# Optimization experiments

Measured on AMD Instinct MI355X. Metric: run time of the kernel, lower is better.

## Reference

```python
import jax, jax.numpy as jnp
import numpy as np

N = 100000   # nodes
E = 1250000  # edges
G = 64       # graphs in batch
F_IN, H, NT, GT = 29, 64, 6, 4
L = 4        # num GCN layers


def setup_inputs() -> dict:
    key = jax.random.key(0)
    ks = jax.random.split(key, 14)
    s_in = 1.0 / np.sqrt(F_IN)
    s_h = 1.0 / np.sqrt(H)
    return {
        "x": jax.random.normal(ks[0], (N, F_IN), dtype=jnp.float32),
        "edge_index": jax.random.randint(ks[1], (2, E), 0, N, dtype=jnp.int64),
        "batch": jnp.sort(jax.random.randint(ks[2], (N,), 0, G, dtype=jnp.int64)),
        "encW": jax.random.uniform(ks[3], (F_IN, H), jnp.float32, -s_in, s_in),
        "encb": jax.random.uniform(ks[4], (H,), jnp.float32, -s_in, s_in),
        "convW": jax.random.uniform(ks[5], (L, H, H), jnp.float32, -s_h, s_h),
        "convb": jax.random.uniform(ks[6], (L, H), jnp.float32, -s_h, s_h),
        "nodeW": jax.random.uniform(ks[7], (H, NT), jnp.float32, -s_h, s_h),
        "nodeb": jax.random.uniform(ks[8], (NT,), jnp.float32, -s_h, s_h),
        "g1W": jax.random.uniform(ks[9], (H, H), jnp.float32, -s_h, s_h),
        "g1b": jax.random.uniform(ks[10], (H,), jnp.float32, -s_h, s_h),
        "g2W": jax.random.uniform(ks[11], (H, GT), jnp.float32, -s_h, s_h),
        "g2b": jax.random.uniform(ks[12], (GT,), jnp.float32, -s_h, s_h),
    }


def reference(x, edge_index, batch, encW, encb, convW, convb, nodeW, nodeb, g1W, g1b, g2W, g2b):
    # GCNConv with self-loops and symmetric normalization (PyG defaults)
    loop = jnp.arange(N, dtype=edge_index.dtype)
    row = jnp.concatenate([edge_index[0], loop])  # senders
    col = jnp.concatenate([edge_index[1], loop])  # receivers
    deg = jax.ops.segment_sum(jnp.ones_like(col, dtype=x.dtype), col, num_segments=N)
    dis = jnp.where(deg > 0, deg ** -0.5, 0.0)
    norm = (dis[row] * dis[col])[:, None]  # [E+N, 1]

    h = jax.nn.relu(x @ encW + encb)
    for i in range(L):
        hw = h @ convW[i]  # transform then propagate
        agg = jax.ops.segment_sum(hw[row] * norm, col, num_segments=N)
        h = jax.nn.relu(agg + convb[i])

    pred_node = h @ nodeW + nodeb

    counts = jax.ops.segment_sum(jnp.ones((N,), x.dtype), batch, num_segments=G)
    gemb = jax.ops.segment_sum(h, batch, num_segments=G) / jnp.maximum(counts, 1.0)[:, None]
    pred_global = jax.nn.relu(gemb @ g1W + g1b) @ g2W + g2b
    return (pred_node, pred_global)
```

## Files before the change

### kernel.cpp

```cpp
#include <hip/hip_runtime.h>
#include <hip/hip_fp16.h>

#define N_NODES 100000
#define N_EDGES 1250000
#define N_GRAPHS 64
#define F_INN 29
#define HD 64
#define NT 6
#define GT 4
#define NLAYERS 4
#define RECS_CAP 3000000
#define NBLK 1563
#define NBUK 782
#define HGRID 256

typedef __attribute__((ext_vector_type(8))) _Float16 f16x8;
typedef __attribute__((ext_vector_type(4))) float f32x4;


__global__ void hist1(const int* __restrict__ col, int* __restrict__ ghistT, int E) {
    __shared__ int lh[NBUK];
    int tid = threadIdx.x, b = blockIdx.x;
    for (int i = tid; i < NBUK; i += 256) lh[i] = 0;
    __syncthreads();
    for (int e = b * 256 + tid; e < E; e += HGRID * 256) atomicAdd(&lh[col[e] >> 7], 1);
    __syncthreads();
    for (int i = tid; i < NBUK; i += 256) ghistT[i * 256 + b] = lh[i];
}

__global__ void hist_colscan(int* __restrict__ ghistT, int* __restrict__ tot) {
    __shared__ int wsum[4];
    int k = blockIdx.x, tid = threadIdx.x;
    int v = ghistT[k * 256 + tid];
    int incl = v;
    int lane = tid & 63;
    #pragma unroll
    for (int off = 1; off < 64; off <<= 1) {
        int t = __shfl_up(incl, (unsigned)off, 64);
        if (lane >= off) incl += t;
    }
    if (lane == 63) wsum[tid >> 6] = incl;
    __syncthreads();
    int woff = 0;
    for (int w = 0; w < (tid >> 6); ++w) woff += wsum[w];
    ghistT[k * 256 + tid] = woff + incl - v;
    if (tid == 255) tot[k] = woff + incl;
}

__global__ void scan1(const int* __restrict__ in, int* __restrict__ out,
                      int* __restrict__ bsums, int n) {
    __shared__ int wsum[4];
    int tid = threadIdx.x;
    int base = blockIdx.x * 1024 + tid * 4;
    int v0 = (base + 0 < n) ? in[base + 0] : 0;
    int v1 = (base + 1 < n) ? in[base + 1] : 0;
    int v2 = (base + 2 < n) ? in[base + 2] : 0;
    int v3 = (base + 3 < n) ? in[base + 3] : 0;
    int tsum = v0 + v1 + v2 + v3;
    int incl = tsum;
    int lane = tid & 63;
    #pragma unroll
    for (int off = 1; off < 64; off <<= 1) {
        int t = __shfl_up(incl, (unsigned)off, 64);
        if (lane >= off) incl += t;
    }
    if (lane == 63) wsum[tid >> 6] = incl;
    __syncthreads();
    int woff = 0;
    for (int w = 0; w < (tid >> 6); ++w) woff += wsum[w];
    int run = woff + incl - tsum;
    if (base + 0 < n) out[base + 0] = run; run += v0;
    if (base + 1 < n) out[base + 1] = run; run += v1;
    if (base + 2 < n) out[base + 2] = run; run += v2;
    if (base + 3 < n) out[base + 3] = run;
    if (tid == 255) bsums[blockIdx.x] = woff + incl;
}

__global__ void scan2(int* __restrict__ bsums, int nb) {
    __shared__ int s[256];
    int tid = threadIdx.x;
    int v = (tid < nb) ? bsums[tid] : 0;
    s[tid] = v;
    __syncthreads();
    #pragma unroll
    for (int off = 1; off < 256; off <<= 1) {
        int t = (tid >= off) ? s[tid - off] : 0;
        __syncthreads();
        s[tid] += t;
        __syncthreads();
    }
    if (tid < nb) bsums[tid] = s[tid] - v;
}

__global__ void scan3(int* __restrict__ out, const int* __restrict__ bsums, int n) {
    int i = blockIdx.x * blockDim.x + threadIdx.x;
    if (i < n) out[i] += bsums[i >> 10];
}

__global__ void scatter_buckets(const int* __restrict__ row, const int* __restrict__ col,
                                const int* __restrict__ ghistT, const int* __restrict__ boff,
                                unsigned* __restrict__ bke, int E) {
    __shared__ int cur[NBUK];
    int tid = threadIdx.x, b = blockIdx.x;
    for (int i = tid; i < NBUK; i += 256) cur[i] = ghistT[i * 256 + b] + boff[i];
    __syncthreads();
    for (int e = b * 256 + tid; e < E; e += HGRID * 256) {
        int c = col[e];
        int pos = atomicAdd(&cur[c >> 7], 1);
        bke[pos] = (unsigned)row[e] | ((unsigned)(c & 127) << 25);
    }
}

__global__ void bucket_count(const unsigned* __restrict__ bke, const int* __restrict__ boff,
                             int* __restrict__ cnt16, float* __restrict__ dis, int E) {
    __shared__ int lc[128];
    int k = blockIdx.x, tid = threadIdx.x;
    if (tid < 128) lc[tid] = 0;
    __syncthreads();
    int s = boff[k];
    int t = (k == NBUK - 1) ? E : boff[k + 1];
    for (int i = s + tid; i < t; i += 256) atomicAdd(&lc[bke[i] >> 25], 1);
    __syncthreads();
    if (tid < 128) {
        int node = k * 128 + tid;
        if (node < N_NODES) {
            int c = lc[tid];
            cnt16[node] = (c + 15) & ~15;
            dis[node] = rsqrtf((float)(c + 1));
        }
    }
}

__global__ void bucket_fill(const unsigned* __restrict__ bke, const int* __restrict__ boff,
                            const int* __restrict__ offs, int* __restrict__ srcs, int E) {
    __shared__ int offsL[128];
    __shared__ int cur[128];
    int k = blockIdx.x, tid = threadIdx.x;
    if (tid < 128) {
        int node = k * 128 + tid;
        offsL[tid] = (node < N_NODES) ? offs[node] : 0;
        cur[tid] = 0;
    }
    __syncthreads();
    int s = boff[k];
    int t = (k == NBUK - 1) ? E : boff[k + 1];
    for (int i = s + tid; i < t; i += 256) {
        unsigned u = bke[i];
        int l = u >> 25;
        int r = atomicAdd(&cur[l], 1);
        srcs[offsL[l] + r] = (int)(u & 0x01FFFFFFu);
    }
    __syncthreads();
    if (tid < 128) {
        int node = k * 128 + tid;
        if (node < N_NODES) {
            int c = cur[tid];
            int c16 = (c + 15) & ~15;
            int base = offsL[tid];
            for (int p = base + c; p < base + c16; ++p) srcs[p] = N_NODES;
        }
    }
}

__global__ void zero_pad_row(__half* __restrict__ h1, __half* __restrict__ h2) {
    int t = threadIdx.x;
    if (t < HD) h1[(size_t)N_NODES * HD + t] = __float2half_rn(0.f);
    else if (t < 2 * HD) h2[(size_t)N_NODES * HD + (t - HD)] = __float2half_rn(0.f);
}

__global__ void graph_bounds(const int* __restrict__ batch, int* __restrict__ start, int n) {
    int i = blockIdx.x * blockDim.x + threadIdx.x;
    if (i >= n) return;
    int b = batch[i];
    if (i == 0) {
        for (int g = 0; g <= b; ++g) start[g] = 0;
    } else {
        int pb = batch[i - 1];
        if (pb != b) for (int g = pb + 1; g <= b; ++g) start[g] = i;
    }
    if (i == n - 1) {
        for (int g = b + 1; g <= N_GRAPHS; ++g) start[g] = n;
    }
}

__global__ void prepack_W(const float* __restrict__ convW, uint4* __restrict__ wfrag) {
    int layer = blockIdx.x;
    const float* W = convW + (size_t)layer * HD * HD;
    uint4* out = wfrag + (size_t)layer * 512;
    for (int s = threadIdx.x; s < 512; s += 256) {
        int jt = s >> 7, ks = (s >> 6) & 1, l = s & 63;
        int j = jt * 16 + (l & 15);
        int k0 = ks * 32 + (l >> 4) * 8;
        __align__(16) __half hh[8];
        #pragma unroll
        for (int i = 0; i < 8; ++i) hh[i] = __float2half_rn(W[(size_t)(k0 + i) * HD + j]);
        out[s] = *reinterpret_cast<const uint4*>(hh);
    }
}


__global__ void encoder_kernel(const float* __restrict__ x, const float* __restrict__ W,
                               const float* __restrict__ b, const float* __restrict__ dis,
                               __half* __restrict__ ht, int n) {
    __shared__ float Ws[F_INN * HD];
    __shared__ float bs[HD];
    __shared__ float xs[16 * F_INN];
    int tid = threadIdx.x;
    for (int i = tid; i < F_INN * HD; i += 256) Ws[i] = W[i];
    if (tid < HD) bs[tid] = b[tid];
    int n0 = blockIdx.x * 16;
    for (int i = tid; i < 16 * F_INN; i += 256) {
        int nn = n0 + i / F_INN;
        xs[i] = (nn < n) ? x[(size_t)nn * F_INN + (i % F_INN)] : 0.f;
    }
    __syncthreads();
    #pragma unroll
    for (int it = 0; it < 4; ++it) {
        int l = it * 4 + (tid >> 6);
        int j = tid & 63;
        int nn = n0 + l;
        if (nn < n) {
            float a = bs[j];
            #pragma unroll
            for (int k = 0; k < F_INN; ++k) a = fmaf(xs[l * F_INN + k], Ws[k * HD + j], a);
            ht[(size_t)nn * HD + j] = __float2half_rn(dis[nn] * fmaxf(a, 0.f));
        }
    }
}

__device__ __forceinline__ float4 cvtrow(uint2 u) {
    float2 a = __half22float2(*reinterpret_cast<const __half2*>(&u.x));
    float2 b = __half22float2(*reinterpret_cast<const __half2*>(&u.y));
    return make_float4(a.x, a.y, b.x, b.y);
}

#define ROW16(src) (*reinterpret_cast<const uint2*>(&ht[(size_t)(src) * HD + fh]))
#define H2(u) (*reinterpret_cast<const __half2*>(&(u)))
#define ACC4T(r0, r1, r2, r3) { \
    __half2 ax = __hadd2(__hadd2(H2(r0.x), H2(r1.x)), __hadd2(H2(r2.x), H2(r3.x))); \
    __half2 ay = __hadd2(__hadd2(H2(r0.y), H2(r1.y)), __hadd2(H2(r2.y), H2(r3.y))); \
    float2 fx = __half22float2(ax); \
    float2 fy = __half22float2(ay); \
    acc.x += fx.x; acc.y += fx.y; acc.z += fy.x; acc.w += fy.y; }

__global__ void layer_kernel(const __half* __restrict__ ht,
                             const int* __restrict__ offs, const int* __restrict__ cnt16,
                             const int4* __restrict__ srcs4,
                             const float* __restrict__ dis,
                             const uint4* __restrict__ wfragL, const float* __restrict__ bias,
                             __half* __restrict__ hout, int scaleOut) {
    __shared__ uint4 WfS[512];
    __shared__ __half aggS[64 * 72];
    __shared__ int offsS[64];
    __shared__ int cntS[64];
    __shared__ float disS[64];
    int tid = threadIdx.x;
    int b = blockIdx.x;
    WfS[tid] = wfragL[tid];
    WfS[tid + 256] = wfragL[tid + 256];
    if (tid < 64) {
        int d = b * 64 + tid;
        if (d < N_NODES) {
            offsS[tid] = offs[d];
            cntS[tid] = cnt16[d];
            disS[tid] = dis[d];
        } else {
            offsS[tid] = offs[N_NODES - 1] + cnt16[N_NODES - 1];
            cntS[tid] = 0;
            disS[tid] = 0.f;
        }
    }
    __syncthreads();

    int wave = tid >> 6;
    int lane = tid & 63;
    int q = lane >> 4;
    int fh = (lane & 15) * 4;

    int l0 = wave * 16 + q * 4;
    int s = offsS[l0];
    int e = offsS[l0 + 3] + cntS[l0 + 3];
    int dcur = l0;
    int nb = offsS[l0] + cntS[l0];
    float4 acc = {0.f, 0.f, 0.f, 0.f};

    auto flush = [&](int d) {
        int nodeD = b * 64 + d;
        float4 sf = cvtrow(*reinterpret_cast<const uint2*>(
            &ht[(size_t)min(nodeD, N_NODES) * HD + fh]));
        acc.x += sf.x; acc.y += sf.y; acc.z += sf.z; acc.w += sf.w;
        __half2 h0 = __floats2half2_rn(acc.x, acc.y);
        __half2 h1 = __floats2half2_rn(acc.z, acc.w);
        uint2 w;
        w.x = *(unsigned*)&h0;
        w.y = *(unsigned*)&h1;
        *reinterpret_cast<uint2*>(&aggS[d * 72 + fh]) = w;
        acc = make_float4(0.f, 0.f, 0.f, 0.f);
    };

    for (int p = s; p < e; p += 16) {
        while (p >= nb) {
            flush(dcur);
            ++dcur;
            nb = offsS[dcur] + cntS[dcur];
        }
        int base = p >> 2;
        int4 e0 = srcs4[base + 0];
        int4 e1 = srcs4[base + 1];
        int4 e2 = srcs4[base + 2];
        int4 e3 = srcs4[base + 3];
        uint2 r0 = ROW16(e0.x), r1 = ROW16(e0.y), r2 = ROW16(e0.z), r3 = ROW16(e0.w);
        uint2 r4 = ROW16(e1.x), r5 = ROW16(e1.y), r6 = ROW16(e1.z), r7 = ROW16(e1.w);
        uint2 r8 = ROW16(e2.x), r9 = ROW16(e2.y), r10 = ROW16(e2.z), r11 = ROW16(e2.w);
        uint2 r12 = ROW16(e3.x), r13 = ROW16(e3.y), r14 = ROW16(e3.z), r15 = ROW16(e3.w);
        ACC4T(r0, r1, r2, r3);
        ACC4T(r4, r5, r6, r7);
        ACC4T(r8, r9, r10, r11);
        ACC4T(r12, r13, r14, r15);
    }
    while (dcur <= l0 + 3) {
        flush(dcur);
        ++dcur;
    }
    __syncthreads();

    f32x4 c0 = {0.f, 0.f, 0.f, 0.f}, c1 = c0, c2 = c0, c3 = c0;
    #pragma unroll
    for (int ks = 0; ks < 2; ++ks) {
        f16x8 bf = *reinterpret_cast<const f16x8*>(&WfS[(wave * 2 + ks) * 64 + lane]);
        f16x8 a0 = *reinterpret_cast<const f16x8*>(&aggS[(0 * 16 + (lane & 15)) * 72 + ks * 32 + (lane >> 4) * 8]);
        c0 = __builtin_amdgcn_mfma_f32_16x16x32_f16(a0, bf, c0, 0, 0, 0);
        f16x8 a1 = *reinterpret_cast<const f16x8*>(&aggS[(1 * 16 + (lane & 15)) * 72 + ks * 32 + (lane >> 4) * 8]);
        c1 = __builtin_amdgcn_mfma_f32_16x16x32_f16(a1, bf, c1, 0, 0, 0);
        f16x8 a2 = *reinterpret_cast<const f16x8*>(&aggS[(2 * 16 + (lane & 15)) * 72 + ks * 32 + (lane >> 4) * 8]);
        c2 = __builtin_amdgcn_mfma_f32_16x16x32_f16(a2, bf, c2, 0, 0, 0);
        f16x8 a3 = *reinterpret_cast<const f16x8*>(&aggS[(3 * 16 + (lane & 15)) * 72 + ks * 32 + (lane >> 4) * 8]);
        c3 = __builtin_amdgcn_mfma_f32_16x16x32_f16(a3, bf, c3, 0, 0, 0);
    }
    int j = wave * 16 + (lane & 15);
    float bj = bias[j];
    #pragma unroll
    for (int nt = 0; nt < 4; ++nt) {
        f32x4 c = (nt == 0) ? c0 : (nt == 1) ? c1 : (nt == 2) ? c2 : c3;
        #pragma unroll
        for (int i = 0; i < 4; ++i) {
            int rl = nt * 16 + (lane >> 4) * 4 + i;
            int node = b * 64 + rl;
            if (node < N_NODES) {
                float dn = disS[rl];
                float o = fmaxf(fmaf(dn, c[i], bj), 0.f);
                if (scaleOut) o *= dn;
                hout[(size_t)node * HD + j] = __float2half_rn(o);
            }
        }
    }
}

__global__ void node_head16(const __half* __restrict__ h, const float* __restrict__ W,
                            const float* __restrict__ b, float* __restrict__ out, int n) {
    __shared__ float Ws[HD * NT];
    __shared__ float bs[NT];
    __shared__ float hs[32 * 65];
    int tid = threadIdx.x;
    for (int i = tid; i < HD * NT; i += 256) Ws[i] = W[i];
    if (tid < NT) bs[tid] = b[tid];
    int n0 = blockIdx.x * 32;
    const unsigned* hrow = reinterpret_cast<const unsigned*>(&h[(size_t)n0 * HD]);
    for (int i = tid; i < 32 * HD / 2; i += 256) {
        unsigned u = hrow[i];
        float2 f = __half22float2(*reinterpret_cast<const __half2*>(&u));
        int el = i * 2;
        int row = el >> 6, colc = el & 63;
        hs[row * 65 + colc] = f.x;
        hs[row * 65 + colc + 1] = f.y;
    }
    __syncthreads();
    int l = tid >> 3, t = tid & 7;
    int nn = n0 + l;
    if (nn < n && t < NT) {
        float a = bs[t];
        #pragma unroll
        for (int k = 0; k < HD; ++k) a = fmaf(hs[l * 65 + k], Ws[k * NT + t], a);
        out[(size_t)nn * NT + t] = a;
    }
}

__global__ void pool16(const __half* __restrict__ h, const int* __restrict__ start,
                       float* __restrict__ gpart) {
    __shared__ float red[4][HD];
    int g = blockIdx.x >> 2, q = blockIdx.x & 3;
    int s0 = start[g], e0 = start[g + 1];
    int len = e0 - s0;
    int qs = s0 + (len * q) / 4;
    int qe = s0 + (len * (q + 1)) / 4;
    int wave = threadIdx.x >> 6, lane = threadIdx.x & 63;
    float acc = 0.f;
    for (int r = qs + wave; r < qe; r += 4) acc += __half2float(h[(size_t)r * HD + lane]);
    red[wave][lane] = acc;
    __syncthreads();
    if (wave == 0)
        gpart[(size_t)blockIdx.x * HD + lane] =
            red[0][lane] + red[1][lane] + red[2][lane] + red[3][lane];
}

__global__ void global_head(const float* __restrict__ gpart, const int* __restrict__ start,
                            const float* __restrict__ g1W, const float* __restrict__ g1b,
                            const float* __restrict__ g2W, const float* __restrict__ g2b,
                            float* __restrict__ out) {
    __shared__ float rS[HD];
    int g = blockIdx.x;
    int j = threadIdx.x;
    int cnt = start[g + 1] - start[g];
    float inv = 1.f / fmaxf((float)cnt, 1.f);
    rS[j] = (gpart[(size_t)(4 * g + 0) * HD + j] + gpart[(size_t)(4 * g + 1) * HD + j] +
             gpart[(size_t)(4 * g + 2) * HD + j] + gpart[(size_t)(4 * g + 3) * HD + j]) * inv;
    __syncthreads();
    float a = g1b[j];
    #pragma unroll
    for (int k = 0; k < HD; ++k) a = fmaf(rS[k], g1W[k * HD + j], a);
    a = fmaxf(a, 0.f);
    float o0 = a * g2W[j * GT + 0];
    float o1 = a * g2W[j * GT + 1];
    float o2 = a * g2W[j * GT + 2];
    float o3 = a * g2W[j * GT + 3];
    #pragma unroll
    for (int off = 1; off < 64; off <<= 1) {
        o0 += __shfl_xor(o0, off, 64);
        o1 += __shfl_xor(o1, off, 64);
        o2 += __shfl_xor(o2, off, 64);
        o3 += __shfl_xor(o3, off, 64);
    }
    if (j == 0) {
        out[g * GT + 0] = o0 + g2b[0];
        out[g * GT + 1] = o1 + g2b[1];
        out[g * GT + 2] = o2 + g2b[2];
        out[g * GT + 3] = o3 + g2b[3];
    }
}


extern "C" void kernel_launch(void* const* d_in, const int* in_sizes, int n_in,
                              void* d_out, int out_size, void* d_ws, size_t ws_size,
                              hipStream_t stream) {
    const float* x    = (const float*)d_in[0];
    const int*   ei   = (const int*)d_in[1];
    const int*   batch= (const int*)d_in[2];
    const float* encW = (const float*)d_in[3];
    const float* encb = (const float*)d_in[4];
    const float* convW= (const float*)d_in[5];
    const float* convb= (const float*)d_in[6];
    const float* nodeW= (const float*)d_in[7];
    const float* nodeb= (const float*)d_in[8];
    const float* g1W  = (const float*)d_in[9];
    const float* g1b  = (const float*)d_in[10];
    const float* g2W  = (const float*)d_in[11];
    const float* g2b  = (const float*)d_in[12];
    float* out = (float*)d_out;

    const int N = N_NODES, E = N_EDGES;

    char* ws = (char*)d_ws;
    size_t off = 0;
    auto alloc = [&](size_t bytes) -> void* {
        void* p = ws + off;
        off += (bytes + 255) & ~(size_t)255;
        return p;
    };
    int*    ghistT = (int*)alloc((size_t)NBUK * 256 * 4);
    int*    tot    = (int*)alloc((size_t)NBUK * 4);
    int*    boff   = (int*)alloc((size_t)NBUK * 4);
    unsigned* bke  = (unsigned*)alloc((size_t)E * 4);
    int*    offs   = (int*)alloc((size_t)N * 4);
    int*    cnt16  = (int*)alloc((size_t)N * 4);
    float*  dis    = (float*)alloc((size_t)N * 4);
    int*    bsums  = (int*)alloc(256 * 4);
    int*    start  = (int*)alloc((size_t)(N_GRAPHS + 1) * 4);
    float*  gpart  = (float*)alloc((size_t)N_GRAPHS * 4 * HD * 4);
    uint4*  wfrag  = (uint4*)alloc((size_t)NLAYERS * 512 * 16);
    int*    srcs   = (int*)alloc((size_t)RECS_CAP * 4);
    __half* ht1    = (__half*)alloc((size_t)(N + 1) * HD * 2);
    __half* ht2    = (__half*)alloc((size_t)(N + 1) * HD * 2);

    const int B = 256;
    hist1<<<HGRID, 256, 0, stream>>>(ei + E, ghistT, E);
    hist_colscan<<<NBUK, 256, 0, stream>>>(ghistT, tot);
    scan1<<<1, 256, 0, stream>>>(tot, boff, bsums, NBUK);
    scatter_buckets<<<HGRID, 256, 0, stream>>>(ei, ei + E, ghistT, boff, bke, E);
    bucket_count<<<NBUK, 256, 0, stream>>>(bke, boff, cnt16, dis, E);
    int nb1 = (N + 1023) / 1024;
    scan1<<<nb1, 256, 0, stream>>>(cnt16, offs, bsums, N);
    scan2<<<1, 256, 0, stream>>>(bsums, nb1);
    scan3<<<(N + B - 1) / B, B, 0, stream>>>(offs, bsums, N);
    bucket_fill<<<NBUK, 256, 0, stream>>>(bke, boff, offs, srcs, E);
    zero_pad_row<<<1, 256, 0, stream>>>(ht1, ht2);
    graph_bounds<<<(N + B - 1) / B, B, 0, stream>>>(batch, start, N);
    prepack_W<<<NLAYERS, 256, 0, stream>>>(convW, wfrag);

    encoder_kernel<<<(N + 15) / 16, 256, 0, stream>>>(x, encW, encb, dis, ht1, N);

    __half* hin = ht1;
    __half* hot = ht2;
    for (int i = 0; i < NLAYERS; ++i) {
        layer_kernel<<<NBLK, 256, 0, stream>>>(hin, offs, cnt16, (const int4*)srcs, dis,
                                               wfrag + (size_t)i * 512,
                                               convb + (size_t)i * HD,
                                               hot, (i < NLAYERS - 1) ? 1 : 0);
        __half* t = hin; hin = hot; hot = t;
    }

    node_head16<<<(N + 31) / 32, 256, 0, stream>>>(hin, nodeW, nodeb, out, N);
    pool16<<<N_GRAPHS * 4, 256, 0, stream>>>(hin, start, gpart);
    global_head<<<N_GRAPHS, 64, 0, stream>>>(gpart, start, g1W, g1b, g2W, g2b, out + (size_t)N * NT);
}
```

Before: 256.2 us.

## Merge setup kernels, replace node-offset scan with per-bucket scan, prefetch self rows

Cuts the launch count by folding independent small kernels into shared launches that branch on block index: weight prepack, pad-row zeroing and graph bounds join the histogram, the encoder joins the bucket fill, and the node head joins pooling. The three-pass node-offset scan is replaced by per-bucket totals computed in bucket_count, one small scan over buckets, and a local in-block scan inside the fill. The layer kernel now loads each block's self-loop rows into shared memory up front, so flush no longer does a scattered global read. The trade-off is more complex heterogeneous kernels and higher shared-memory use per block.

```diff
diff --git a/kernel.cpp b/kernel.cpp
--- a/kernel.cpp
+++ b/kernel.cpp
@@ -13,19 +13,56 @@
 #define NBLK 1563
 #define NBUK 782
 #define HGRID 256
+#define GB_BLOCKS 391
+#define ENC_BLOCKS 6250
+#define NH_BLOCKS 3125
 
 typedef __attribute__((ext_vector_type(8))) _Float16 f16x8;
 typedef __attribute__((ext_vector_type(4))) float f32x4;
 
-
-__global__ void hist1(const int* __restrict__ col, int* __restrict__ ghistT, int E) {
+__global__ void hist1_misc(const int* __restrict__ col, int* __restrict__ ghistT, int E,
+                           const float* __restrict__ convW, uint4* __restrict__ wfrag,
+                           __half* __restrict__ ht1, __half* __restrict__ ht2,
+                           const int* __restrict__ batch, int* __restrict__ start) {
     __shared__ int lh[NBUK];
     int tid = threadIdx.x, b = blockIdx.x;
-    for (int i = tid; i < NBUK; i += 256) lh[i] = 0;
-    __syncthreads();
-    for (int e = b * 256 + tid; e < E; e += HGRID * 256) atomicAdd(&lh[col[e] >> 7], 1);
-    __syncthreads();
-    for (int i = tid; i < NBUK; i += 256) ghistT[i * 256 + b] = lh[i];
+    if (b < HGRID) {
+        for (int i = tid; i < NBUK; i += 256) lh[i] = 0;
+        __syncthreads();
+        for (int e = b * 256 + tid; e < E; e += HGRID * 256) atomicAdd(&lh[col[e] >> 7], 1);
+        __syncthreads();
+        for (int i = tid; i < NBUK; i += 256) ghistT[i * 256 + b] = lh[i];
+    } else if (b < HGRID + 4) {
+        int layer = b - HGRID;
+        const float* W = convW + (size_t)layer * HD * HD;
+        uint4* out = wfrag + (size_t)layer * 512;
+        for (int s = tid; s < 512; s += 256) {
+            int jt = s >> 7, ks = (s >> 6) & 1, l = s & 63;
+            int j = jt * 16 + (l & 15);
+            int k0 = ks * 32 + (l >> 4) * 8;
+            __align__(16) __half hh[8];
+            #pragma unroll
+            for (int i = 0; i < 8; ++i) hh[i] = __float2half_rn(W[(size_t)(k0 + i) * HD + j]);
+            out[s] = *reinterpret_cast<const uint4*>(hh);
+        }
+    } else if (b == HGRID + 4) {
+        if (tid < HD) ht1[(size_t)N_NODES * HD + tid] = __float2half_rn(0.f);
+        else if (tid < 2 * HD) ht2[(size_t)N_NODES * HD + (tid - HD)] = __float2half_rn(0.f);
+    } else {
+        int i = (b - HGRID - 5) * 256 + tid;
+        if (i < N_NODES) {
+            int bb = batch[i];
+            if (i == 0) {
+                for (int g = 0; g <= bb; ++g) start[g] = 0;
+            } else {
+                int pb = batch[i - 1];
+                if (pb != bb) for (int g = pb + 1; g <= bb; ++g) start[g] = i;
+            }
+            if (i == N_NODES - 1) {
+                for (int g = bb + 1; g <= N_GRAPHS; ++g) start[g] = N_NODES;
+            }
+        }
+    }
 }
 
 __global__ void hist_colscan(int* __restrict__ ghistT, int* __restrict__ tot) {
@@ -76,27 +113,6 @@
     if (tid == 255) bsums[blockIdx.x] = woff + incl;
 }
 
-__global__ void scan2(int* __restrict__ bsums, int nb) {
-    __shared__ int s[256];
-    int tid = threadIdx.x;
-    int v = (tid < nb) ? bsums[tid] : 0;
-    s[tid] = v;
-    __syncthreads();
-    #pragma unroll
-    for (int off = 1; off < 256; off <<= 1) {
-        int t = (tid >= off) ? s[tid - off] : 0;
-        __syncthreads();
-        s[tid] += t;
-        __syncthreads();
-    }
-    if (tid < nb) bsums[tid] = s[tid] - v;
-}
-
-__global__ void scan3(int* __restrict__ out, const int* __restrict__ bsums, int n) {
-    int i = blockIdx.x * blockDim.x + threadIdx.x;
-    if (i < n) out[i] += bsums[i >> 10];
-}
-
 __global__ void scatter_buckets(const int* __restrict__ row, const int* __restrict__ col,
                                 const int* __restrict__ ghistT, const int* __restrict__ boff,
                                 unsigned* __restrict__ bke, int E) {
@@ -112,8 +128,10 @@
 }
 
 __global__ void bucket_count(const unsigned* __restrict__ bke, const int* __restrict__ boff,
-                             int* __restrict__ cnt16, float* __restrict__ dis, int E) {
+                             int* __restrict__ cnt16, float* __restrict__ dis,
+                             int* __restrict__ btot, int E) {
     __shared__ int lc[128];
+    __shared__ int red[2];
     int k = blockIdx.x, tid = threadIdx.x;
     if (tid < 128) lc[tid] = 0;
     __syncthreads();
@@ -121,112 +139,105 @@
     int t = (k == NBUK - 1) ? E : boff[k + 1];
     for (int i = s + tid; i < t; i += 256) atomicAdd(&lc[bke[i] >> 25], 1);
     __syncthreads();
+    int c16 = 0;
     if (tid < 128) {
         int node = k * 128 + tid;
         if (node < N_NODES) {
             int c = lc[tid];
-            cnt16[node] = (c + 15) & ~15;
+            c16 = (c + 15) & ~15;
+            cnt16[node] = c16;
             dis[node] = rsqrtf((float)(c + 1));
         }
-    }
-}
-
-__global__ void bucket_fill(const unsigned* __restrict__ bke, const int* __restrict__ boff,
-                            const int* __restrict__ offs, int* __restrict__ srcs, int E) {
-    __shared__ int offsL[128];
-    __shared__ int cur[128];
-    int k = blockIdx.x, tid = threadIdx.x;
-    if (tid < 128) {
-        int node = k * 128 + tid;
-        offsL[tid] = (node < N_NODES) ? offs[node] : 0;
-        cur[tid] = 0;
-    }
-    __syncthreads();
-    int s = boff[k];
-    int t = (k == NBUK - 1) ? E : boff[k + 1];
-    for (int i = s + tid; i < t; i += 256) {
-        unsigned u = bke[i];
-        int l = u >> 25;
-        int r = atomicAdd(&cur[l], 1);
-        srcs[offsL[l] + r] = (int)(u & 0x01FFFFFFu);
-    }
-    __syncthreads();
-    if (tid < 128) {
-        int node = k * 128 + tid;
-        if (node < N_NODES) {
-            int c = cur[tid];
-            int c16 = (c + 15) & ~15;
-            int base = offsL[tid];
-            for (int p = base + c; p < base + c16; ++p) srcs[p] = N_NODES;
-        }
-    }
-}
-
-__global__ void zero_pad_row(__half* __restrict__ h1, __half* __restrict__ h2) {
-    int t = threadIdx.x;
-    if (t < HD) h1[(size_t)N_NODES * HD + t] = __float2half_rn(0.f);
-    else if (t < 2 * HD) h2[(size_t)N_NODES * HD + (t - HD)] = __float2half_rn(0.f);
-}
-
-__global__ void graph_bounds(const int* __restrict__ batch, int* __restrict__ start, int n) {
-    int i = blockIdx.x * blockDim.x + threadIdx.x;
-    if (i >= n) return;
-    int b = batch[i];
-    if (i == 0) {
-        for (int g = 0; g <= b; ++g) start[g] = 0;
+        int sum = c16;
+        #pragma unroll
+        for (int off = 1; off < 64; off <<= 1) sum += __shfl_xor(sum, off, 64);
+        if ((tid & 63) == 0) red[tid >> 6] = sum;
+    }
+    __syncthreads();
+    if (tid == 0) btot[k] = red[0] + red[1];
+}
+
+__global__ void fill_enc(const unsigned* __restrict__ bke, const int* __restrict__ boff,
+                         const int* __restrict__ bbase, const int* __restrict__ cnt16,
+                         int* __restrict__ offs, int* __restrict__ srcs, int E,
+                         const float* __restrict__ x, const float* __restrict__ encW,
+                         const float* __restrict__ encb, const float* __restrict__ dis,
+                         __half* __restrict__ ht) {
+    int tid = threadIdx.x;
+    int b = blockIdx.x;
+    if (b < NBUK) {
+        __shared__ int offsL[128];
+        __shared__ int cur[128];
+        __shared__ int wtot[2];
+        int k = b;
+        int v = 0, incl = 0;
+        if (tid < 128) {
+            int node = k * 128 + tid;
+            v = (node < N_NODES) ? cnt16[node] : 0;
+            incl = v;
+            int lane = tid & 63;
+            #pragma unroll
+            for (int off = 1; off < 64; off <<= 1) {
+                int t = __shfl_up(incl, (unsigned)off, 64);
+                if (lane >= off) incl += t;
+            }
+            if (lane == 63) wtot[tid >> 6] = incl;
+        }
+        __syncthreads();
+        if (tid < 128) {
+            int w0 = (tid >= 64) ? wtot[0] : 0;
+            int node = k * 128 + tid;
+            int o = bbase[k] + w0 + incl - v;
+            offsL[tid] = o;
+            cur[tid] = 0;
+            if (node < N_NODES) offs[node] = o;
+        }
+        __syncthreads();
+        int s = boff[k];
+        int t = (k == NBUK - 1) ? E : boff[k + 1];
+        for (int i = s + tid; i < t; i += 256) {
+            unsigned u = bke[i];
+            int l = u >> 25;
+            int r = atomicAdd(&cur[l], 1);
+            srcs[offsL[l] + r] = (int)(u & 0x01FFFFFFu);
+        }
+        __syncthreads();
+        if (tid < 128) {
+            int node = k * 128 + tid;
+            if (node < N_NODES) {
+                int c = cur[tid];
+                int c16 = (c + 15) & ~15;
+                int base = offsL[tid];
+                for (int p = base + c; p < base + c16; ++p) srcs[p] = N_NODES;
+            }
+        }
     } else {
-        int pb = batch[i - 1];
-        if (pb != b) for (int g = pb + 1; g <= b; ++g) start[g] = i;
-    }
-    if (i == n - 1) {
-        for (int g = b + 1; g <= N_GRAPHS; ++g) start[g] = n;
-    }
-}
-
-__global__ void prepack_W(const float* __restrict__ convW, uint4* __restrict__ wfrag) {
-    int layer = blockIdx.x;
-    const float* W = convW + (size_t)layer * HD * HD;
-    uint4* out = wfrag + (size_t)layer * 512;
-    for (int s = threadIdx.x; s < 512; s += 256) {
-        int jt = s >> 7, ks = (s >> 6) & 1, l = s & 63;
-        int j = jt * 16 + (l & 15);
-        int k0 = ks * 32 + (l >> 4) * 8;
-        __align__(16) __half hh[8];
+        __shared__ float Ws[F_INN * HD];
+        __shared__ float bs[HD];
+        __shared__ float xs[16 * F_INN];
+        for (int i = tid; i < F_INN * HD; i += 256) Ws[i] = encW[i];
+        if (tid < HD) bs[tid] = encb[tid];
+        int n0 = (b - NBUK) * 16;
+        for (int i = tid; i < 16 * F_INN; i += 256) {
+            int nn = n0 + i / F_INN;
+            xs[i] = (nn < N_NODES) ? x[(size_t)nn * F_INN + (i % F_INN)] : 0.f;
+        }
+        __syncthreads();
         #pragma unroll
-        for (int i = 0; i < 8; ++i) hh[i] = __float2half_rn(W[(size_t)(k0 + i) * HD + j]);
-        out[s] = *reinterpret_cast<const uint4*>(hh);
-    }
-}
-
-
-__global__ void encoder_kernel(const float* __restrict__ x, const float* __restrict__ W,
-                               const float* __restrict__ b, const float* __restrict__ dis,
-                               __half* __restrict__ ht, int n) {
-    __shared__ float Ws[F_INN * HD];
-    __shared__ float bs[HD];
-    __shared__ float xs[16 * F_INN];
-    int tid = threadIdx.x;
-    for (int i = tid; i < F_INN * HD; i += 256) Ws[i] = W[i];
-    if (tid < HD) bs[tid] = b[tid];
-    int n0 = blockIdx.x * 16;
-    for (int i = tid; i < 16 * F_INN; i += 256) {
-        int nn = n0 + i / F_INN;
-        xs[i] = (nn < n) ? x[(size_t)nn * F_INN + (i % F_INN)] : 0.f;
-    }
-    __syncthreads();
-    #pragma unroll
-    for (int it = 0; it < 4; ++it) {
-        int l = it * 4 + (tid >> 6);
-        int j = tid & 63;
-        int nn = n0 + l;
-        if (nn < n) {
-            float a = bs[j];
-            #pragma unroll
-            for (int k = 0; k < F_INN; ++k) a = fmaf(xs[l * F_INN + k], Ws[k * HD + j], a);
-            ht[(size_t)nn * HD + j] = __float2half_rn(dis[nn] * fmaxf(a, 0.f));
-        }
-    }
-}
+        for (int it = 0; it < 4; ++it) {
+            int l = it * 4 + (tid >> 6);
+            int j = tid & 63;
+            int nn = n0 + l;
+            if (nn < N_NODES) {
+                float a = bs[j];
+                #pragma unroll
+                for (int k = 0; k < F_INN; ++k) a = fmaf(xs[l * F_INN + k], Ws[k * HD + j], a);
+                ht[(size_t)nn * HD + j] = __float2half_rn(dis[nn] * fmaxf(a, 0.f));
+            }
+        }
+    }
+}
+
 
 __device__ __forceinline__ float4 cvtrow(uint2 u) {
     float2 a = __half22float2(*reinterpret_cast<const __half2*>(&u.x));
@@ -278,6 +289,13 @@
     int fh = (lane & 15) * 4;
 
     int l0 = wave * 16 + q * 4;
+    {
+        int nbase = b * 64 + l0;
+        *reinterpret_cast<uint2*>(&aggS[(l0 + 0) * 72 + fh]) = ROW16(min(nbase + 0, N_NODES));
+        *reinterpret_cast<uint2*>(&aggS[(l0 + 1) * 72 + fh]) = ROW16(min(nbase + 1, N_NODES));
+        *reinterpret_cast<uint2*>(&aggS[(l0 + 2) * 72 + fh]) = ROW16(min(nbase + 2, N_NODES));
+        *reinterpret_cast<uint2*>(&aggS[(l0 + 3) * 72 + fh]) = ROW16(min(nbase + 3, N_NODES));
+    }
     int s = offsS[l0];
     int e = offsS[l0 + 3] + cntS[l0 + 3];
     int dcur = l0;
@@ -285,9 +303,8 @@
     float4 acc = {0.f, 0.f, 0.f, 0.f};
 
     auto flush = [&](int d) {
-        int nodeD = b * 64 + d;
-        float4 sf = cvtrow(*reinterpret_cast<const uint2*>(
-            &ht[(size_t)min(nodeD, N_NODES) * HD + fh]));
+        uint2 sv = *reinterpret_cast<uint2*>(&aggS[d * 72 + fh]);
+        float4 sf = cvtrow(sv);
         acc.x += sf.x; acc.y += sf.y; acc.z += sf.z; acc.w += sf.w;
         __half2 h0 = __floats2half2_rn(acc.x, acc.y);
         __half2 h1 = __floats2half2_rn(acc.z, acc.w);
@@ -356,51 +373,53 @@
     }
 }
 
-__global__ void node_head16(const __half* __restrict__ h, const float* __restrict__ W,
-                            const float* __restrict__ b, float* __restrict__ out, int n) {
-    __shared__ float Ws[HD * NT];
-    __shared__ float bs[NT];
-    __shared__ float hs[32 * 65];
+__global__ void heads_kernel(const __half* __restrict__ h, const float* __restrict__ W,
+                             const float* __restrict__ bb, float* __restrict__ out,
+                             const int* __restrict__ start, float* __restrict__ gpart) {
     int tid = threadIdx.x;
-    for (int i = tid; i < HD * NT; i += 256) Ws[i] = W[i];
-    if (tid < NT) bs[tid] = b[tid];
-    int n0 = blockIdx.x * 32;
-    const unsigned* hrow = reinterpret_cast<const unsigned*>(&h[(size_t)n0 * HD]);
-    for (int i = tid; i < 32 * HD / 2; i += 256) {
-        unsigned u = hrow[i];
-        float2 f = __half22float2(*reinterpret_cast<const __half2*>(&u));
-        int el = i * 2;
-        int row = el >> 6, colc = el & 63;
-        hs[row * 65 + colc] = f.x;
-        hs[row * 65 + colc + 1] = f.y;
-    }
-    __syncthreads();
-    int l = tid >> 3, t = tid & 7;
-    int nn = n0 + l;
-    if (nn < n && t < NT) {
-        float a = bs[t];
-        #pragma unroll
-        for (int k = 0; k < HD; ++k) a = fmaf(hs[l * 65 + k], Ws[k * NT + t], a);
-        out[(size_t)nn * NT + t] = a;
-    }
-}
-
-__global__ void pool16(const __half* __restrict__ h, const int* __restrict__ start,
-                       float* __restrict__ gpart) {
-    __shared__ float red[4][HD];
-    int g = blockIdx.x >> 2, q = blockIdx.x & 3;
-    int s0 = start[g], e0 = start[g + 1];
-    int len = e0 - s0;
-    int qs = s0 + (len * q) / 4;
-    int qe = s0 + (len * (q + 1)) / 4;
-    int wave = threadIdx.x >> 6, lane = threadIdx.x & 63;
-    float acc = 0.f;
-    for (int r = qs + wave; r < qe; r += 4) acc += __half2float(h[(size_t)r * HD + lane]);
-    red[wave][lane] = acc;
-    __syncthreads();
-    if (wave == 0)
-        gpart[(size_t)blockIdx.x * HD + lane] =
-            red[0][lane] + red[1][lane] + red[2][lane] + red[3][lane];
+    int b = blockIdx.x;
+    if (b < NH_BLOCKS) {
+        __shared__ float Ws[HD * NT];
+        __shared__ float bs[NT];
+        __shared__ float hs[32 * 65];
+        for (int i = tid; i < HD * NT; i += 256) Ws[i] = W[i];
+        if (tid < NT) bs[tid] = bb[tid];
+        int n0 = b * 32;
+        const unsigned* hrow = reinterpret_cast<const unsigned*>(&h[(size_t)n0 * HD]);
+        for (int i = tid; i < 32 * HD / 2; i += 256) {
+            unsigned u = hrow[i];
+            float2 f = __half22float2(*reinterpret_cast<const __half2*>(&u));
+            int el = i * 2;
+            int row = el >> 6, colc = el & 63;
+            hs[row * 65 + colc] = f.x;
+            hs[row * 65 + colc + 1] = f.y;
+        }
+        __syncthreads();
+        int l = tid >> 3, t = tid & 7;
+        int nn = n0 + l;
+        if (nn < N_NODES && t < NT) {
+            float a = bs[t];
+            #pragma unroll
+            for (int k = 0; k < HD; ++k) a = fmaf(hs[l * 65 + k], Ws[k * NT + t], a);
+            out[(size_t)nn * NT + t] = a;
+        }
+    } else {
+        __shared__ float red[4][HD];
+        int pb = b - NH_BLOCKS;
+        int g = pb >> 2, q = pb & 3;
+        int s0 = start[g], e0 = start[g + 1];
+        int len = e0 - s0;
+        int qs = s0 + (len * q) / 4;
+        int qe = s0 + (len * (q + 1)) / 4;
+        int wave = tid >> 6, lane = tid & 63;
+        float acc = 0.f;
+        for (int r = qs + wave; r < qe; r += 4) acc += __half2float(h[(size_t)r * HD + lane]);
+        red[wave][lane] = acc;
+        __syncthreads();
+        if (wave == 0)
+            gpart[(size_t)pb * HD + lane] =
+                red[0][lane] + red[1][lane] + red[2][lane] + red[3][lane];
+    }
 }
 
 __global__ void global_head(const float* __restrict__ gpart, const int* __restrict__ start,
@@ -469,6 +488,8 @@
     int*    ghistT = (int*)alloc((size_t)NBUK * 256 * 4);
     int*    tot    = (int*)alloc((size_t)NBUK * 4);
     int*    boff   = (int*)alloc((size_t)NBUK * 4);
+    int*    btot   = (int*)alloc((size_t)NBUK * 4);
+    int*    bbase  = (int*)alloc((size_t)NBUK * 4);
     unsigned* bke  = (unsigned*)alloc((size_t)E * 4);
     int*    offs   = (int*)alloc((size_t)N * 4);
     int*    cnt16  = (int*)alloc((size_t)N * 4);
@@ -481,22 +502,15 @@
     __half* ht1    = (__half*)alloc((size_t)(N + 1) * HD * 2);
     __half* ht2    = (__half*)alloc((size_t)(N + 1) * HD * 2);
 
-    const int B = 256;
-    hist1<<<HGRID, 256, 0, stream>>>(ei + E, ghistT, E);
+    hist1_misc<<<HGRID + 5 + GB_BLOCKS, 256, 0, stream>>>(ei + E, ghistT, E, convW, wfrag,
+                                                          ht1, ht2, batch, start);
     hist_colscan<<<NBUK, 256, 0, stream>>>(ghistT, tot);
     scan1<<<1, 256, 0, stream>>>(tot, boff, bsums, NBUK);
     scatter_buckets<<<HGRID, 256, 0, stream>>>(ei, ei + E, ghistT, boff, bke, E);
-    bucket_count<<<NBUK, 256, 0, stream>>>(bke, boff, cnt16, dis, E);
-    int nb1 = (N + 1023) / 1024;
-    scan1<<<nb1, 256, 0, stream>>>(cnt16, offs, bsums, N);
-    scan2<<<1, 256, 0, stream>>>(bsums, nb1);
-    scan3<<<(N + B - 1) / B, B, 0, stream>>>(offs, bsums, N);
-    bucket_fill<<<NBUK, 256, 0, stream>>>(bke, boff, offs, srcs, E);
-    zero_pad_row<<<1, 256, 0, stream>>>(ht1, ht2);
-    graph_bounds<<<(N + B - 1) / B, B, 0, stream>>>(batch, start, N);
-    prepack_W<<<NLAYERS, 256, 0, stream>>>(convW, wfrag);
-
-    encoder_kernel<<<(N + 15) / 16, 256, 0, stream>>>(x, encW, encb, dis, ht1, N);
+    bucket_count<<<NBUK, 256, 0, stream>>>(bke, boff, cnt16, dis, btot, E);
+    scan1<<<1, 256, 0, stream>>>(btot, bbase, bsums, NBUK);
+    fill_enc<<<NBUK + ENC_BLOCKS, 256, 0, stream>>>(bke, boff, bbase, cnt16, offs, srcs, E,
+                                                    x, encW, encb, dis, ht1);
 
     __half* hin = ht1;
     __half* hot = ht2;
@@ -508,7 +522,7 @@
         __half* t = hin; hin = hot; hot = t;
     }
 
-    node_head16<<<(N + 31) / 32, 256, 0, stream>>>(hin, nodeW, nodeb, out, N);
-    pool16<<<N_GRAPHS * 4, 256, 0, stream>>>(hin, start, gpart);
+    heads_kernel<<<NH_BLOCKS + N_GRAPHS * 4, 256, 0, stream>>>(hin, nodeW, nodeb, out,
+                                                               start, gpart);
     global_head<<<N_GRAPHS, 64, 0, stream>>>(gpart, start, g1W, g1b, g2W, g2b, out + (size_t)N * NT);
 }
```

Result: faster. 233.4 us (-8.9%).
